# Optimization experiments

Hardware: AMD Instinct MI355X
Metric: run time of the kernel (lower is better)

Reference implementation:

```python
import jax, jax.numpy as jnp
import numpy as np

B, S, HID = 4, 2048, 2048
NH, NKV = 8, 1
HD = HID // NH  # 256
G = NH // NKV   # queries per kv head
ROPE_THETA = 10000.0
NEG_INF = -1e9


def setup_inputs() -> dict:
    key = jax.random.key(0)
    ks = jax.random.split(key, 4)
    x = jax.random.normal(ks[0], (B, S, HID), jnp.float32)
    qkv_dim = (NH + 2 * NKV) * HD
    w_qkv = jax.random.normal(ks[1], (HID, qkv_dim), jnp.float32) * (HID ** -0.5)
    b_qkv = jnp.zeros((qkv_dim,), jnp.float32)
    w_o = jax.random.normal(ks[2], (NH * HD, HID), jnp.float32) * ((NH * HD) ** -0.5)
    b_o = jnp.zeros((HID,), jnp.float32)
    # rotary table: cos/sin of position*inv_freq, interleaved-pair convention
    inv_freq = 1.0 / (ROPE_THETA ** (jnp.arange(0, HD, 2, dtype=jnp.float32) / HD))
    ang = jnp.outer(jnp.arange(S, dtype=jnp.float32), inv_freq)  # [S, HD/2]
    freqs_cis = jnp.stack([jnp.cos(ang), jnp.sin(ang)], axis=-1)  # [S, HD/2, 2]
    causal = jnp.tril(jnp.ones((S, S), bool))
    mask = jnp.where(causal, 0.0, NEG_INF).astype(jnp.float32)[None, None]  # [1,1,S,S]
    return dict(x=x, w_qkv=w_qkv, b_qkv=b_qkv, w_o=w_o, b_o=b_o,
                freqs_cis=freqs_cis, mask=mask)


def _rope(t, cos, sin):
    # t: [B,S,H,D]; cos/sin: [1,S,1,D/2]; interleaved complex pairs
    tp = t.reshape(*t.shape[:-1], -1, 2)
    r, i = tp[..., 0], tp[..., 1]
    out = jnp.stack([r * cos - i * sin, r * sin + i * cos], axis=-1)
    return out.reshape(t.shape)


def reference(x, w_qkv, b_qkv, w_o, b_o, freqs_cis, mask):
    b, s, _ = x.shape
    qkv = x @ w_qkv + b_qkv
    q, k, v = jnp.split(qkv, [NH * HD, NH * HD + NKV * HD], axis=-1)
    q = q.reshape(b, s, NH, HD)
    k = k.reshape(b, s, NKV, HD)
    v = v.reshape(b, s, NKV, HD)
    cos = freqs_cis[..., 0][None, :, None, :]
    sin = freqs_cis[..., 1][None, :, None, :]
    q = _rope(q, cos, sin)
    k = _rope(k, cos, sin)
    # GQA: head h attends with kv group h // G (same layout as repeat_interleave)
    qh = q.transpose(0, 2, 1, 3).reshape(b, NKV, G, s, HD)  # [B,KV,G,S,D]
    kh = k.transpose(0, 2, 1, 3)                            # [B,KV,S,D]
    vh = v.transpose(0, 2, 1, 3)
    scores = jnp.einsum('bkgqd,bksd->bkgqs', qh, kh) * (HD ** -0.5)
    scores = scores + mask[:, :, None]  # broadcast over group dim
    attn = jax.nn.softmax(scores.astype(jnp.float32), axis=-1).astype(q.dtype)
    out = jnp.einsum('bkgqs,bksd->bkgqd', attn, vh)         # [B,KV,G,S,D]
    out = out.reshape(b, NH, s, HD).transpose(0, 2, 1, 3).reshape(b, s, NH * HD)
    return out @ w_o + b_o
```

## Files before the change

kernel.cpp:

```cpp
#include <hip/hip_runtime.h>
#include <hip/hip_bf16.h>

#define B_ 4
#define S_ 2048
#define HID_ 2048
#define NH_ 8
#define HD_ 256
#define QKVN 2560

typedef unsigned short u16;
typedef unsigned long long ull;
typedef __attribute__((ext_vector_type(4))) float f32x4;
typedef __attribute__((ext_vector_type(16))) float f32x16;
typedef __attribute__((ext_vector_type(8))) short bf16x8;

__device__ __forceinline__ float bf2f(u16 u) {
  union { unsigned int i; float f; } v; v.i = ((unsigned int)u) << 16; return v.f;
}
__device__ __forceinline__ u16 f2bf(float f) {
  union { unsigned int i; float f; } v; v.f = f;
  unsigned int r = v.i + 0x7fffu + ((v.i >> 16) & 1u);
  return (u16)(r >> 16);
}

__global__ void cast_f32_bf16(const float* __restrict__ in, u16* __restrict__ out, int n8) {
  int i = blockIdx.x * blockDim.x + threadIdx.x;
  int stride = gridDim.x * blockDim.x;
  for (; i < n8; i += stride) {
    const float4* p = (const float4*)(in + (size_t)i * 8);
    float4 a = p[0], b = p[1];
    u16 o[8] = {f2bf(a.x), f2bf(a.y), f2bf(a.z), f2bf(a.w),
                f2bf(b.x), f2bf(b.y), f2bf(b.z), f2bf(b.w)};
    *(uint4*)(out + (size_t)i * 8) = *(const uint4*)o;
  }
}

__global__ void transpose_cast(const float* __restrict__ in, u16* __restrict__ out, int R, int C) {
  __shared__ float t[32][33];
  int c0 = blockIdx.x * 32, r0 = blockIdx.y * 32;
  int tx = threadIdx.x, ty = threadIdx.y;
#pragma unroll
  for (int i = 0; i < 4; ++i)
    t[ty + i * 8][tx] = in[(size_t)(r0 + ty + i * 8) * C + c0 + tx];
  __syncthreads();
#pragma unroll
  for (int i = 0; i < 4; ++i)
    out[(size_t)(c0 + ty + i * 8) * R + r0 + tx] = f2bf(t[tx][ty + i * 8]);
}

__global__ void transpose_bf16(const u16* __restrict__ in, u16* __restrict__ out, int R, int C) {
  __shared__ u16 t[32][33];
  in += (size_t)blockIdx.z * R * C;
  out += (size_t)blockIdx.z * R * C;
  int c0 = blockIdx.x * 32, r0 = blockIdx.y * 32;
  int tx = threadIdx.x, ty = threadIdx.y;
#pragma unroll
  for (int i = 0; i < 4; ++i)
    t[ty + i * 8][tx] = in[(size_t)(r0 + ty + i * 8) * C + c0 + tx];
  __syncthreads();
#pragma unroll
  for (int i = 0; i < 4; ++i)
    out[(size_t)(c0 + ty + i * 8) * R + r0 + tx] = t[tx][ty + i * 8];
}

#define BAR() __builtin_amdgcn_s_barrier()
#define PRIO1() __builtin_amdgcn_s_setprio(1)
#define PRIO0() __builtin_amdgcn_s_setprio(0)
#define SB0() __builtin_amdgcn_sched_barrier(0)
#define WVM(n)                                                                                    \
  do {                                                                                            \
    SB0();                                                                                        \
    asm volatile("s_waitcnt vmcnt(" #n ")" ::: "memory");                                         \
    SB0();                                                                                        \
  } while (0)

#define STG(mat, b0, h, T, ldsb)                                                                  \
  do {                                                                                            \
    _Pragma("unroll") for (int q = 0; q < 2; ++q) {                                               \
      int idx = q * 512 + tid;                                                                    \
      int rl = idx >> 3, gp = idx & 7;                                                            \
      const u16* s = (mat) + (size_t)((b0) + (h) * 128 + rl) * K + (T) * 64 +                     \
                     ((gp ^ (rl & 7)) << 3);                                                      \
      __builtin_amdgcn_global_load_lds((const __attribute__((address_space(1))) void*)s,          \
          (__attribute__((address_space(3))) void*)((ldsb) + (h) * 8192 + idx * 8), 16, 0, 0);    \
    }                                                                                             \
  } while (0)

#define LOAD_A(buf, mib)                                                                          \
  _Pragma("unroll") for (int mi = 0; mi < 4; ++mi)                                                \
  _Pragma("unroll") for (int ks = 0; ks < 2; ++ks)                                                \
    af[mi][ks] = *(const bf16x8*)((buf) + (wr * 128 + ((mib) + mi) * 16 + l15) * 64 +             \
                                  (((ks * 4 + lg) ^ (l15 & 7)) << 3));

#define LOAD_B(buf, nib)                                                                          \
  _Pragma("unroll") for (int ni = 0; ni < 2; ++ni)                                                \
  _Pragma("unroll") for (int ks = 0; ks < 2; ++ks)                                                \
    bfr[(nib) + ni][ks] = *(const bf16x8*)((buf) + (wc * 64 + ((nib) + ni) * 16 + l15) * 64 +     \
                                           (((ks * 4 + lg) ^ (l15 & 7)) << 3));

#define MFMA16(accb, nib)                                                                         \
  _Pragma("unroll") for (int mi = 0; mi < 4; ++mi)                                                \
  _Pragma("unroll") for (int ni = 0; ni < 2; ++ni)                                                \
  _Pragma("unroll") for (int ks = 0; ks < 2; ++ks)                                                \
    acc[(accb) + mi][(nib) + ni] = __builtin_amdgcn_mfma_f32_16x16x32_bf16(                       \
        af[mi][ks], bfr[(nib) + ni][ks], acc[(accb) + mi][(nib) + ni], 0, 0, 0);

template <bool OUT_F32>
__global__ __launch_bounds__(512, 2) void gemm256(const u16* __restrict__ A, const u16* __restrict__ BT,
                                                  const float* __restrict__ bias, void* __restrict__ Cout,
                                                  int M, int N, int K) {
  __shared__ u16 Asm[2][16384];
  __shared__ u16 Bsm[2][16384];
  int nwg = gridDim.x;
  int bid = (int)blockIdx.x;
  bid = (bid & 7) * (nwg >> 3) + (bid >> 3);
  int ntn = N >> 8;
  int m0 = (bid / ntn) << 8, n0 = (bid % ntn) << 8;
  int tid = threadIdx.x, w = tid >> 6, lane = tid & 63;
  int wr = w >> 2, wc = w & 3;
  int l15 = lane & 15, lg = lane >> 4;
  int NT = K >> 6;
  u16* A0b = &Asm[0][0]; u16* A1b = &Asm[1][0];
  u16* B0b = &Bsm[0][0]; u16* B1b = &Bsm[1][0];
  f32x4 acc[8][4] = {};
  bf16x8 af[4][2], bfr[4][2];

  STG(A, m0, 0, 0, A0b); STG(A, m0, 1, 0, A0b);
  STG(BT, n0, 0, 0, B0b); STG(BT, n0, 1, 0, B0b);
  STG(A, m0, 0, 1, A1b); STG(BT, n0, 0, 1, B1b);
  WVM(0);
  BAR();

  for (int T = 0; T + 2 < NT; T += 2) {
    LOAD_A(A0b, 0); LOAD_B(B0b, 0);
    STG(A, m0, 1, T + 1, A1b);
    BAR(); PRIO1(); MFMA16(0, 0); PRIO0(); BAR();
    LOAD_B(B0b, 2);
    STG(BT, n0, 1, T + 1, B1b);
    BAR(); PRIO1(); MFMA16(0, 2); PRIO0(); BAR();
    LOAD_A(A0b, 4);
    STG(BT, n0, 0, T + 2, B0b);
    BAR(); PRIO1(); MFMA16(4, 0); PRIO0(); BAR();
    STG(A, m0, 0, T + 2, A0b);
    WVM(4);
    BAR(); PRIO1(); MFMA16(4, 2); PRIO0(); BAR();
    LOAD_A(A1b, 0); LOAD_B(B1b, 0);
    STG(A, m0, 1, T + 2, A0b);
    BAR(); PRIO1(); MFMA16(0, 0); PRIO0(); BAR();
    LOAD_B(B1b, 2);
    STG(BT, n0, 1, T + 2, B0b);
    BAR(); PRIO1(); MFMA16(0, 2); PRIO0(); BAR();
    LOAD_A(A1b, 4);
    STG(BT, n0, 0, T + 3, B1b);
    BAR(); PRIO1(); MFMA16(4, 0); PRIO0(); BAR();
    STG(A, m0, 0, T + 3, A1b);
    WVM(4);
    BAR(); PRIO1(); MFMA16(4, 2); PRIO0(); BAR();
  }
  {
    int T = NT - 2;
    LOAD_A(A0b, 0); LOAD_B(B0b, 0);
    STG(A, m0, 1, T + 1, A1b);
    BAR(); PRIO1(); MFMA16(0, 0); PRIO0(); BAR();
    LOAD_B(B0b, 2);
    STG(BT, n0, 1, T + 1, B1b);
    BAR(); PRIO1(); MFMA16(0, 2); PRIO0(); BAR();
    LOAD_A(A0b, 4);
    BAR(); PRIO1(); MFMA16(4, 0); PRIO0(); BAR();
    WVM(0);
    BAR(); PRIO1(); MFMA16(4, 2); PRIO0(); BAR();
    LOAD_A(A1b, 0); LOAD_B(B1b, 0);
    BAR(); PRIO1(); MFMA16(0, 0); PRIO0(); BAR();
    LOAD_B(B1b, 2);
    BAR(); PRIO1(); MFMA16(0, 2); PRIO0(); BAR();
    LOAD_A(A1b, 4);
    BAR(); PRIO1(); MFMA16(4, 0); PRIO0(); BAR();
    PRIO1(); MFMA16(4, 2); PRIO0();
  }
#pragma unroll
  for (int mi = 0; mi < 8; ++mi) {
    int mrow = m0 + wr * 128 + mi * 16 + lg * 4;
#pragma unroll
    for (int ni = 0; ni < 4; ++ni) {
      int col = n0 + wc * 64 + ni * 16 + l15;
      float bv = bias[col];
#pragma unroll
      for (int j = 0; j < 4; ++j) {
        float v = acc[mi][ni][j] + bv;
        if (OUT_F32)
          ((float*)Cout)[(size_t)(mrow + j) * N + col] = v;
        else
          ((u16*)Cout)[(size_t)(mrow + j) * N + col] = f2bf(v);
      }
    }
  }
}

__global__ void rope_scatter(const u16* __restrict__ qkv, const float* __restrict__ freqs,
                             u16* __restrict__ qo, u16* __restrict__ ko, u16* __restrict__ vo) {
  const int per_row = QKVN / 8;
  const int total = B_ * S_ * per_row;
  int i = blockIdx.x * blockDim.x + threadIdx.x;
  int stride = gridDim.x * blockDim.x;
  for (; i < total; i += stride) {
    int m = i / per_row;
    int n8 = (i - m * per_row) * 8;
    int b = m >> 11, s = m & 2047;
    uint4 raw = *(const uint4*)(qkv + (size_t)m * QKVN + n8);
    const u16* u = (const u16*)&raw;
    if (n8 < 2304) {
      int d = (n8 < 2048) ? (n8 & 255) : (n8 - 2048);
      float scl = (n8 < 2048) ? (0.0625f * 1.44269504f) : 1.0f;
      const float* fp = freqs + ((size_t)s * 128 + (d >> 1)) * 2;
      float4 f0 = *(const float4*)fp;
      float4 f1 = *(const float4*)(fp + 4);
      float fc[8] = {f0.x, f0.y, f0.z, f0.w, f1.x, f1.y, f1.z, f1.w};
      u16 o[8];
#pragma unroll
      for (int p = 0; p < 4; ++p) {
        float r = bf2f(u[2 * p]), im = bf2f(u[2 * p + 1]);
        float c = fc[2 * p], sn = fc[2 * p + 1];
        o[2 * p] = f2bf((r * c - im * sn) * scl);
        o[2 * p + 1] = f2bf((r * sn + im * c) * scl);
      }
      u16* dst;
      if (n8 < 2048) {
        dst = qo + (size_t)m * 2048 + n8;
      } else {
        dst = ko + (((size_t)m) << 8) + d;
      }
      *(uint4*)dst = *(const uint4*)o;
    } else {
      int d = n8 - 2304;
      *(uint4*)(vo + (((size_t)m) << 8) + d) = raw;
    }
  }
}

#define STAGE_K(bufofs, kt)                                                                       \
  do {                                                                                            \
    _Pragma("unroll") for (int _p = 0; _p < 4; ++_p) {                                            \
      int _idx = _p * 512 + tid;                                                                  \
      int _row = _idx >> 5, _c = _idx & 31;                                                       \
      const u16* _src = Kp + ((size_t)(b * S_ + (kt) * 64 + _row)) * HD_ +                        \
                        ((_c ^ (_row & 31)) * 8);                                                 \
      __builtin_amdgcn_global_load_lds(                                                           \
          (const __attribute__((address_space(1))) void*)_src,                                    \
          (__attribute__((address_space(3))) void*)(KsBase + (bufofs) + _idx * 8), 16, 0, 0);     \
    }                                                                                             \
  } while (0)

#define STAGE_V(bufofs, kt)                                                                       \
  do {                                                                                            \
    _Pragma("unroll") for (int _p = 0; _p < 4; ++_p) {                                            \
      int _idx = _p * 512 + tid;                                                                  \
      int _r = _idx >> 4, _gp = _idx & 15;                                                        \
      int _g = _gp ^ (_r & 15);                                                                   \
      int _d = _r * 2 + (_g >> 3), _c = _g & 7;                                                   \
      const u16* _src = VTp + ((size_t)(b * 256 + _d)) * S_ + (kt) * 64 + _c * 8;                 \
      __builtin_amdgcn_global_load_lds(                                                           \
          (const __attribute__((address_space(1))) void*)_src,                                    \
          (__attribute__((address_space(3))) void*)(VsBase + (bufofs) + _idx * 8), 16, 0, 0);     \
    }                                                                                             \
  } while (0)

#define FLASH_TAU_BODY(Kbp, Vbp)                                                                  \
  do {                                                                                            \
    int row = tau * 32 + l31;                                                                     \
    f32x16 scv = {};                                                                              \
    __builtin_amdgcn_s_setprio(1);                                                                \
    _Pragma("unroll") for (int st = 0; st < 16; ++st) {                                           \
      bf16x8 kf = *(const bf16x8*)((Kbp) + row * 512 + (((st * 2 + lh) ^ l31) << 4));             \
      scv = __builtin_amdgcn_mfma_f32_32x32x16_bf16(kf, qf[st], scv, 0, 0, 0);                    \
    }                                                                                             \
    __builtin_amdgcn_s_setprio(0);                                                                \
    if (k0 + 31 > t * 32) {                                                                       \
      _Pragma("unroll") for (int jj = 0; jj < 16; ++jj) {                                         \
        int kg = k0 + (jj & 3) + 8 * (jj >> 2) + 4 * lh;                                          \
        if (kg > s_g) scv[jj] = -3.0e38f;                                                         \
      }                                                                                           \
    }                                                                                             \
    float tmax = -3.0e38f;                                                                        \
    _Pragma("unroll") for (int jj = 0; jj < 16; ++jj) tmax = fmaxf(tmax, scv[jj]);                \
    tmax = fmaxf(tmax, __shfl_xor(tmax, 32));                                                     \
    if (!__all(tmax - m_r <= 8.0f)) {                                                             \
      float mnew = fmaxf(m_r, tmax);                                                              \
      float sc = exp2f(m_r - mnew);                                                               \
      l_r *= sc;                                                                                  \
      _Pragma("unroll") for (int dt = 0; dt < 8; ++dt) oacc[dt] *= sc;                            \
      m_r = mnew;                                                                                 \
    }                                                                                             \
    float ts = 0.f;                                                                               \
    unsigned cpk[8];                                                                              \
    _Pragma("unroll") for (int mi = 0; mi < 8; ++mi) {                                            \
      float p0 = exp2f(scv[2 * mi] - m_r);                                                        \
      float p1 = exp2f(scv[2 * mi + 1] - m_r);                                                    \
      ts += p0 + p1;                                                                              \
      cpk[mi] = ((unsigned)f2bf(p1) << 16) | f2bf(p0);                                            \
    }                                                                                             \
    ts += __shfl_xor(ts, 32);                                                                     \
    l_r += ts;                                                                                    \
    asm volatile("v_permlane32_swap_b32 %0, %1" : "+v"(cpk[0]), "+v"(cpk[2]));                    \
    asm volatile("v_permlane32_swap_b32 %0, %1" : "+v"(cpk[1]), "+v"(cpk[3]));                    \
    asm volatile("v_permlane32_swap_b32 %0, %1" : "+v"(cpk[4]), "+v"(cpk[6]));                    \
    asm volatile("v_permlane32_swap_b32 %0, %1" : "+v"(cpk[5]), "+v"(cpk[7]));                    \
    union { unsigned u[4]; bf16x8 v; } pa, pb;                                                    \
    pa.u[0] = cpk[0]; pa.u[1] = cpk[1]; pa.u[2] = cpk[2]; pa.u[3] = cpk[3];                       \
    pb.u[0] = cpk[4]; pb.u[1] = cpk[5]; pb.u[2] = cpk[6]; pb.u[3] = cpk[7];                       \
    __builtin_amdgcn_s_setprio(1);                                                                \
    _Pragma("unroll") for (int dt = 0; dt < 8; ++dt) {                                            \
      int d = dt * 32 + l31;                                                                      \
      int rr = d >> 1;                                                                            \
      int gb = (d & 1) * 8 + tau * 4;                                                             \
      int rx = (rr & 15) << 4;                                                                    \
      bf16x8 va = *(const bf16x8*)((Vbp) + rr * 256 + (((gb + lh) << 4) ^ rx));                   \
      oacc[dt] = __builtin_amdgcn_mfma_f32_32x32x16_bf16(va, pa.v, oacc[dt], 0, 0, 0);            \
      bf16x8 vb2 = *(const bf16x8*)((Vbp) + rr * 256 + (((gb + 2 + lh) << 4) ^ rx));              \
      oacc[dt] = __builtin_amdgcn_mfma_f32_32x32x16_bf16(vb2, pb.v, oacc[dt], 0, 0, 0);           \
    }                                                                                             \
    __builtin_amdgcn_s_setprio(0);                                                                \
  } while (0)

__global__ __launch_bounds__(512, 2) void flash_attn_split(const u16* __restrict__ Qp, const u16* __restrict__ Kp,
                                                           const u16* __restrict__ VTp, u16* __restrict__ P0,
                                                           float* __restrict__ ml0, float* __restrict__ ml1,
                                                           u16* __restrict__ Op) {
  __shared__ u16 Ks[2][64 * 256];
  __shared__ u16 Vs[2][128 * 128];
  int bid = (int)blockIdx.x;
  int b = (bid & 7) >> 1;
  int j = ((bid & 1) << 5) + (bid >> 3);
  int tid = threadIdx.x;
  int w = tid >> 6, l = tid & 63;
  int l31 = l & 31, lh = l >> 5;
  int q_local = w * 32 + l31;
  u16* KsBase = &Ks[0][0];
  u16* VsBase = &Vs[0][0];

  for (int seg = 0; seg < 2; ++seg) {
    int t = seg ? (63 - j) : j;
    int nkv = (t >> 1) + 1;
    int half = (nkv + 1) >> 1;
    int kb = seg ? half : 0;
    int ke = seg ? nkv : half;
    size_t qrow = (size_t)b * 16384 + (size_t)t * 256 + q_local;
    int s_g = t * 32 + (q_local >> 3);
    float* mlbuf = seg ? ml1 : ml0;
    if (kb >= ke) {
      if (lh == 0) { mlbuf[qrow * 2] = -3.0e38f; mlbuf[qrow * 2 + 1] = 0.f; }
      continue;
    }
    bf16x8 qf[16];
    const u16* qp = Qp + qrow * HD_ + lh * 8;
#pragma unroll
    for (int st = 0; st < 16; ++st) qf[st] = *(const bf16x8*)(qp + st * 16);
    f32x16 oacc[8] = {};
    float m_r = -3.0e38f, l_r = 0.f;
    STAGE_K(0, kb);
    STAGE_V(0, kb);
    __syncthreads();
    int cur = 0;
    for (int kt = kb; kt < ke; ++kt) {
      if (kt + 1 < ke) {
        STAGE_K((cur ^ 1) * 16384, kt + 1);
        STAGE_V((cur ^ 1) * 16384, kt + 1);
      }
      const char* Kb = (const char*)(KsBase + cur * 16384);
      const char* Vb = (const char*)(VsBase + cur * 16384);
#pragma unroll
      for (int tau = 0; tau < 2; ++tau) {
        int k0 = kt * 64 + tau * 32;
        if (k0 > t * 32 + 31) break;
        FLASH_TAU_BODY(Kb, Vb);
      }
      __syncthreads();
      cur ^= 1;
    }
    float inv = 1.0f / l_r;
    u16* ob = (seg ? Op : P0) + qrow * 256;
#pragma unroll
    for (int dt = 0; dt < 8; ++dt) {
#pragma unroll
      for (int jj = 0; jj < 4; ++jj) {
        int d0 = dt * 32 + jj * 8 + 4 * lh;
        u16 o4[4];
#pragma unroll
        for (int e = 0; e < 4; ++e) o4[e] = f2bf(oacc[dt][jj * 4 + e] * inv);
        *(ull*)(ob + d0) = *(const ull*)o4;
      }
    }
    if (lh == 0) { mlbuf[qrow * 2] = m_r; mlbuf[qrow * 2 + 1] = l_r; }
  }
}

__global__ __launch_bounds__(256) void combine_parts(const u16* __restrict__ P0, const float* __restrict__ ml0,
                                                     const float* __restrict__ ml1, u16* __restrict__ O) {
  int idx = blockIdx.x * 256 + threadIdx.x;
  int r = idx >> 5;
  int c = (idx & 31) * 8;
  float m0 = ml0[(size_t)r * 2], l0 = ml0[(size_t)r * 2 + 1];
  float m1 = ml1[(size_t)r * 2], l1 = ml1[(size_t)r * 2 + 1];
  float M = fmaxf(m0, m1);
  float w0 = l0 * exp2f(m0 - M), w1 = l1 * exp2f(m1 - M);
  float inv = 1.0f / (w0 + w1);
  w0 *= inv; w1 *= inv;
  uint4 a = *(const uint4*)(P0 + (size_t)r * 256 + c);
  uint4 bq = *(const uint4*)(O + (size_t)r * 256 + c);
  const u16* ua = (const u16*)&a;
  const u16* ub = (const u16*)&bq;
  u16 o[8];
#pragma unroll
  for (int e = 0; e < 8; ++e) o[e] = f2bf(w0 * bf2f(ua[e]) + w1 * bf2f(ub[e]));
  *(uint4*)(O + (size_t)r * 256 + c) = *(const uint4*)o;
}

#define STAGE_K1(kt)                                                                              \
  do {                                                                                            \
    _Pragma("unroll") for (int _p = 0; _p < 4; ++_p) {                                            \
      int _idx = _p * 512 + tid;                                                                  \
      int _row = _idx >> 5, _c = _idx & 31;                                                       \
      const u16* _src = Kp + ((size_t)(b * S_ + (kt) * 64 + _row)) * HD_ +                        \
                        ((_c ^ (_row & 31)) * 8);                                                 \
      __builtin_amdgcn_global_load_lds(                                                           \
          (const __attribute__((address_space(1))) void*)_src,                                    \
          (__attribute__((address_space(3))) void*)(KsBase + _idx * 8), 16, 0, 0);                \
    }                                                                                             \
  } while (0)

#define STAGE_V1(kt)                                                                              \
  do {                                                                                            \
    _Pragma("unroll") for (int _p = 0; _p < 4; ++_p) {                                            \
      int _idx = _p * 512 + tid;                                                                  \
      int _r = _idx >> 4, _gp = _idx & 15;                                                        \
      int _g = _gp ^ (_r & 15);                                                                   \
      int _d = _r * 2 + (_g >> 3), _c = _g & 7;                                                   \
      const u16* _src = VTp + ((size_t)(b * 256 + _d)) * S_ + (kt) * 64 + _c * 8;                 \
      __builtin_amdgcn_global_load_lds(                                                           \
          (const __attribute__((address_space(1))) void*)_src,                                    \
          (__attribute__((address_space(3))) void*)(VsBase + _idx * 8), 16, 0, 0);                \
    }                                                                                             \
  } while (0)

__global__ __launch_bounds__(512, 2) void flash_attn_split4(const u16* __restrict__ Qp, const u16* __restrict__ Kp,
                                                            const u16* __restrict__ VTp,
                                                            u16* __restrict__ P0, u16* __restrict__ P1,
                                                            u16* __restrict__ P2, u16* __restrict__ Op,
                                                            float* __restrict__ ml0, float* __restrict__ ml1,
                                                            float* __restrict__ ml2, float* __restrict__ ml3) {
  __shared__ u16 Ks[64 * 256];
  __shared__ u16 Vs[128 * 128];
  int bid = (int)blockIdx.x;
  int b = (bid & 7) >> 1;
  int rest = ((bid & 1) << 7) | (bid >> 3);
  int t = rest & 63;
  int p = rest >> 6;
  int tid = threadIdx.x;
  int w = tid >> 6, l = tid & 63;
  int l31 = l & 31, lh = l >> 5;
  int q_local = w * 32 + l31;
  u16* KsBase = &Ks[0];
  u16* VsBase = &Vs[0];

  int nkv = (t >> 1) + 1;
  int kb = (nkv * p) >> 2;
  int ke = (nkv * (p + 1)) >> 2;
  size_t qrow = (size_t)b * 16384 + (size_t)t * 256 + q_local;
  int s_g = t * 32 + (q_local >> 3);
  u16* Obuf = (p == 0) ? P0 : (p == 1) ? P1 : (p == 2) ? P2 : Op;
  float* mlbuf = (p == 0) ? ml0 : (p == 1) ? ml1 : (p == 2) ? ml2 : ml3;

  if (kb >= ke) {
    if (lh == 0) { mlbuf[qrow * 2] = -3.0e38f; mlbuf[qrow * 2 + 1] = 0.f; }
    return;
  }

  bf16x8 qf[16];
  const u16* qp = Qp + qrow * HD_ + lh * 8;
#pragma unroll
  for (int st = 0; st < 16; ++st) qf[st] = *(const bf16x8*)(qp + st * 16);
  f32x16 oacc[8] = {};
  float m_r = -3.0e38f, l_r = 0.f;

  STAGE_K1(kb);
  STAGE_V1(kb);
  __syncthreads();
  for (int kt = kb; kt < ke; ++kt) {
#pragma unroll
    for (int tau = 0; tau < 2; ++tau) {
      int k0 = kt * 64 + tau * 32;
      if (k0 > t * 32 + 31) break;
      FLASH_TAU_BODY((const char*)KsBase, (const char*)VsBase);
    }
    __syncthreads();
    if (kt + 1 < ke) {
      STAGE_K1(kt + 1);
      STAGE_V1(kt + 1);
      __syncthreads();
    }
  }

  float inv = 1.0f / l_r;
  u16* ob = Obuf + qrow * 256;
#pragma unroll
  for (int dt = 0; dt < 8; ++dt) {
#pragma unroll
    for (int jj = 0; jj < 4; ++jj) {
      int d0 = dt * 32 + jj * 8 + 4 * lh;
      u16 o4[4];
#pragma unroll
      for (int e = 0; e < 4; ++e) o4[e] = f2bf(oacc[dt][jj * 4 + e] * inv);
      *(ull*)(ob + d0) = *(const ull*)o4;
    }
  }
  if (lh == 0) { mlbuf[qrow * 2] = m_r; mlbuf[qrow * 2 + 1] = l_r; }
}

__global__ __launch_bounds__(256) void combine_parts4(const u16* __restrict__ P0, const u16* __restrict__ P1,
                                                      const u16* __restrict__ P2, const float* __restrict__ ml0,
                                                      const float* __restrict__ ml1, const float* __restrict__ ml2,
                                                      const float* __restrict__ ml3, u16* __restrict__ O) {
  int idx = blockIdx.x * 256 + threadIdx.x;
  int r = idx >> 5;
  int c = (idx & 31) * 8;
  float m0 = ml0[(size_t)r * 2], l0 = ml0[(size_t)r * 2 + 1];
  float m1 = ml1[(size_t)r * 2], l1 = ml1[(size_t)r * 2 + 1];
  float m2 = ml2[(size_t)r * 2], l2 = ml2[(size_t)r * 2 + 1];
  float m3 = ml3[(size_t)r * 2], l3 = ml3[(size_t)r * 2 + 1];
  float M = fmaxf(fmaxf(m0, m1), fmaxf(m2, m3));
  float w0 = l0 * exp2f(m0 - M), w1 = l1 * exp2f(m1 - M);
  float w2 = l2 * exp2f(m2 - M), w3 = l3 * exp2f(m3 - M);
  float inv = 1.0f / (w0 + w1 + w2 + w3);
  w0 *= inv; w1 *= inv; w2 *= inv; w3 *= inv;
  uint4 a0 = *(const uint4*)(P0 + (size_t)r * 256 + c);
  uint4 a1 = *(const uint4*)(P1 + (size_t)r * 256 + c);
  uint4 a2 = *(const uint4*)(P2 + (size_t)r * 256 + c);
  uint4 a3 = *(const uint4*)(O + (size_t)r * 256 + c);
  const u16* u0 = (const u16*)&a0;
  const u16* u1 = (const u16*)&a1;
  const u16* u2 = (const u16*)&a2;
  const u16* u3 = (const u16*)&a3;
  u16 o[8];
#pragma unroll
  for (int e = 0; e < 8; ++e)
    o[e] = f2bf(w0 * bf2f(u0[e]) + w1 * bf2f(u1[e]) + w2 * bf2f(u2[e]) + w3 * bf2f(u3[e]));
  *(uint4*)(O + (size_t)r * 256 + c) = *(const uint4*)o;
}

extern "C" void kernel_launch(void* const* d_in, const int* in_sizes, int n_in,
                              void* d_out, int out_size, void* d_ws, size_t ws_size,
                              hipStream_t stream) {
  const float* x = (const float*)d_in[0];
  const float* w_qkv = (const float*)d_in[1];
  const float* b_qkv = (const float*)d_in[2];
  const float* w_o = (const float*)d_in[3];
  const float* b_o = (const float*)d_in[4];
  const float* freqs = (const float*)d_in[5];

  char* ws = (char*)d_ws;
  u16* xb    = (u16*)ws;
  u16* wqkvT = (u16*)(ws + 33554432);
  u16* woT   = (u16*)(ws + 44040192);
  u16* qkv   = (u16*)(ws + 52428800);
  u16* qall  = (u16*)(ws + 94371840);
  u16* kbuf  = (u16*)(ws + 127926272);
  u16* vbuf  = (u16*)(ws + 132120576);
  u16* part0 = (u16*)(ws + 136314880);
  float* ml0 = (float*)(ws + 169869312);
  float* ml1 = (float*)(ws + 170393600);
  u16* part1 = (u16*)(ws + 170917888);
  u16* part2 = (u16*)(ws + 204472320);
  float* ml2 = (float*)(ws + 33554432);
  float* ml3 = (float*)(ws + 33554432 + 524288);
  u16* vT    = xb;
  u16* attout = qkv;

  bool split4 = (ws_size >= 238026752ULL);

  cast_f32_bf16<<<2048, 256, 0, stream>>>(x, xb, (B_ * S_ * HID_) / 8);
  transpose_cast<<<dim3(QKVN / 32, HID_ / 32), dim3(32, 8), 0, stream>>>(w_qkv, wqkvT, HID_, QKVN);
  transpose_cast<<<dim3(HID_ / 32, HID_ / 32), dim3(32, 8), 0, stream>>>(w_o, woT, HID_, HID_);
  gemm256<false><<<dim3(32 * 10), 512, 0, stream>>>(xb, wqkvT, b_qkv, qkv, B_ * S_, QKVN, HID_);
  rope_scatter<<<2048, 256, 0, stream>>>(qkv, freqs, qall, kbuf, vbuf);
  transpose_bf16<<<dim3(HD_ / 32, S_ / 32, B_), dim3(32, 8), 0, stream>>>(vbuf, vT, S_, HD_);
  if (split4) {
    flash_attn_split4<<<1024, 512, 0, stream>>>(qall, kbuf, vT, part0, part1, part2, attout,
                                                ml0, ml1, ml2, ml3);
    combine_parts4<<<8192, 256, 0, stream>>>(part0, part1, part2, ml0, ml1, ml2, ml3, attout);
  } else {
    flash_attn_split<<<256, 512, 0, stream>>>(qall, kbuf, vT, part0, ml0, ml1, attout);
    combine_parts<<<8192, 256, 0, stream>>>(part0, ml0, ml1, attout);
  }
  gemm256<true><<<dim3(32 * 8), 512, 0, stream>>>(attout, woT, b_o, d_out, B_ * S_, HID_, HID_);
}
```

Before: 464.7 us.

## Replace 4-way KV split attention with 2-way split using smaller 256-thread blocks

```diff
diff --git a/kernel.cpp b/kernel.cpp
--- a/kernel.cpp
+++ b/kernel.cpp
@@ -237,30 +237,31 @@
   }
 }
 
-#define STAGE_K(bufofs, kt)                                                                       \
+
+#define STAGE_K1(kt)                                                                              \
   do {                                                                                            \
-    _Pragma("unroll") for (int _p = 0; _p < 4; ++_p) {                                            \
-      int _idx = _p * 512 + tid;                                                                  \
+    _Pragma("unroll") for (int _p = 0; _p < 8; ++_p) {                                            \
+      int _idx = _p * 256 + tid;                                                                  \
       int _row = _idx >> 5, _c = _idx & 31;                                                       \
       const u16* _src = Kp + ((size_t)(b * S_ + (kt) * 64 + _row)) * HD_ +                        \
                         ((_c ^ (_row & 31)) * 8);                                                 \
       __builtin_amdgcn_global_load_lds(                                                           \
           (const __attribute__((address_space(1))) void*)_src,                                    \
-          (__attribute__((address_space(3))) void*)(KsBase + (bufofs) + _idx * 8), 16, 0, 0);     \
+          (__attribute__((address_space(3))) void*)(KsBase + _idx * 8), 16, 0, 0);                \
     }                                                                                             \
   } while (0)
 
-#define STAGE_V(bufofs, kt)                                                                       \
+#define STAGE_V1(kt)                                                                              \
   do {                                                                                            \
-    _Pragma("unroll") for (int _p = 0; _p < 4; ++_p) {                                            \
-      int _idx = _p * 512 + tid;                                                                  \
+    _Pragma("unroll") for (int _p = 0; _p < 8; ++_p) {                                            \
+      int _idx = _p * 256 + tid;                                                                  \
       int _r = _idx >> 4, _gp = _idx & 15;                                                        \
       int _g = _gp ^ (_r & 15);                                                                   \
       int _d = _r * 2 + (_g >> 3), _c = _g & 7;                                                   \
       const u16* _src = VTp + ((size_t)(b * 256 + _d)) * S_ + (kt) * 64 + _c * 8;                 \
       __builtin_amdgcn_global_load_lds(                                                           \
           (const __attribute__((address_space(1))) void*)_src,                                    \
-          (__attribute__((address_space(3))) void*)(VsBase + (bufofs) + _idx * 8), 16, 0, 0);     \
+          (__attribute__((address_space(3))) void*)(VsBase + _idx * 8), 16, 0, 0);                \
     }                                                                                             \
   } while (0)
 
@@ -274,7 +275,7 @@
       scv = __builtin_amdgcn_mfma_f32_32x32x16_bf16(kf, qf[st], scv, 0, 0, 0);                    \
     }                                                                                             \
     __builtin_amdgcn_s_setprio(0);                                                                \
-    if (k0 + 31 > t * 32) {                                                                       \
+    if (needmask) {                                                                               \
       _Pragma("unroll") for (int jj = 0; jj < 16; ++jj) {                                         \
         int kg = k0 + (jj & 3) + 8 * (jj >> 2) + 4 * lh;                                          \
         if (kg > s_g) scv[jj] = -3.0e38f;                                                         \
@@ -321,31 +322,33 @@
     __builtin_amdgcn_s_setprio(0);                                                                \
   } while (0)
 
-__global__ __launch_bounds__(512, 2) void flash_attn_split(const u16* __restrict__ Qp, const u16* __restrict__ Kp,
+__global__ __launch_bounds__(256, 2) void flash_attn_split(const u16* __restrict__ Qp, const u16* __restrict__ Kp,
                                                            const u16* __restrict__ VTp, u16* __restrict__ P0,
                                                            float* __restrict__ ml0, float* __restrict__ ml1,
                                                            u16* __restrict__ Op) {
-  __shared__ u16 Ks[2][64 * 256];
-  __shared__ u16 Vs[2][128 * 128];
+  __shared__ u16 Ks[64 * 256];
+  __shared__ u16 Vs[128 * 128];
   int bid = (int)blockIdx.x;
   int b = (bid & 7) >> 1;
-  int j = ((bid & 1) << 5) + (bid >> 3);
+  int part = bid & 1;
+  int pair = bid >> 3;
   int tid = threadIdx.x;
   int w = tid >> 6, l = tid & 63;
   int l31 = l & 31, lh = l >> 5;
   int q_local = w * 32 + l31;
-  u16* KsBase = &Ks[0][0];
-  u16* VsBase = &Vs[0][0];
+  u16* KsBase = &Ks[0];
+  u16* VsBase = &Vs[0];
+  float* mlbuf = part ? ml1 : ml0;
 
   for (int seg = 0; seg < 2; ++seg) {
-    int t = seg ? (63 - j) : j;
-    int nkv = (t >> 1) + 1;
+    int t = seg ? (127 - pair) : pair;
+    int nkv = (t >> 2) + 1;
     int half = (nkv + 1) >> 1;
-    int kb = seg ? half : 0;
-    int ke = seg ? nkv : half;
-    size_t qrow = (size_t)b * 16384 + (size_t)t * 256 + q_local;
-    int s_g = t * 32 + (q_local >> 3);
-    float* mlbuf = seg ? ml1 : ml0;
+    int kb = part ? half : 0;
+    int ke = part ? nkv : half;
+    size_t qrow = (size_t)b * 16384 + (size_t)t * 128 + q_local;
+    int s_g = t * 16 + (q_local >> 3);
+    int smin = t * 16, smax = t * 16 + 15;
     if (kb >= ke) {
       if (lh == 0) { mlbuf[qrow * 2] = -3.0e38f; mlbuf[qrow * 2 + 1] = 0.f; }
       continue;
@@ -356,28 +359,28 @@
     for (int st = 0; st < 16; ++st) qf[st] = *(const bf16x8*)(qp + st * 16);
     f32x16 oacc[8] = {};
     float m_r = -3.0e38f, l_r = 0.f;
-    STAGE_K(0, kb);
-    STAGE_V(0, kb);
+
+    STAGE_K1(kb);
+    STAGE_V1(kb);
     __syncthreads();
-    int cur = 0;
     for (int kt = kb; kt < ke; ++kt) {
-      if (kt + 1 < ke) {
-        STAGE_K((cur ^ 1) * 16384, kt + 1);
-        STAGE_V((cur ^ 1) * 16384, kt + 1);
-      }
-      const char* Kb = (const char*)(KsBase + cur * 16384);
-      const char* Vb = (const char*)(VsBase + cur * 16384);
 #pragma unroll
       for (int tau = 0; tau < 2; ++tau) {
         int k0 = kt * 64 + tau * 32;
-        if (k0 > t * 32 + 31) break;
-        FLASH_TAU_BODY(Kb, Vb);
+        if (k0 > smax) break;
+        bool needmask = (k0 + 31 > smin);
+        FLASH_TAU_BODY((const char*)KsBase, (const char*)VsBase);
       }
       __syncthreads();
-      cur ^= 1;
+      if (kt + 1 < ke) {
+        STAGE_K1(kt + 1);
+        STAGE_V1(kt + 1);
+        __syncthreads();
+      }
     }
+
     float inv = 1.0f / l_r;
-    u16* ob = (seg ? Op : P0) + qrow * 256;
+    u16* ob = (part ? Op : P0) + qrow * 256;
 #pragma unroll
     for (int dt = 0; dt < 8; ++dt) {
 #pragma unroll
@@ -414,138 +417,6 @@
   *(uint4*)(O + (size_t)r * 256 + c) = *(const uint4*)o;
 }
 
-#define STAGE_K1(kt)                                                                              \
-  do {                                                                                            \
-    _Pragma("unroll") for (int _p = 0; _p < 4; ++_p) {                                            \
-      int _idx = _p * 512 + tid;                                                                  \
-      int _row = _idx >> 5, _c = _idx & 31;                                                       \
-      const u16* _src = Kp + ((size_t)(b * S_ + (kt) * 64 + _row)) * HD_ +                        \
-                        ((_c ^ (_row & 31)) * 8);                                                 \
-      __builtin_amdgcn_global_load_lds(                                                           \
-          (const __attribute__((address_space(1))) void*)_src,                                    \
-          (__attribute__((address_space(3))) void*)(KsBase + _idx * 8), 16, 0, 0);                \
-    }                                                                                             \
-  } while (0)
-
-#define STAGE_V1(kt)                                                                              \
-  do {                                                                                            \
-    _Pragma("unroll") for (int _p = 0; _p < 4; ++_p) {                                            \
-      int _idx = _p * 512 + tid;                                                                  \
-      int _r = _idx >> 4, _gp = _idx & 15;                                                        \
-      int _g = _gp ^ (_r & 15);                                                                   \
-      int _d = _r * 2 + (_g >> 3), _c = _g & 7;                                                   \
-      const u16* _src = VTp + ((size_t)(b * 256 + _d)) * S_ + (kt) * 64 + _c * 8;                 \
-      __builtin_amdgcn_global_load_lds(                                                           \
-          (const __attribute__((address_space(1))) void*)_src,                                    \
-          (__attribute__((address_space(3))) void*)(VsBase + _idx * 8), 16, 0, 0);                \
-    }                                                                                             \
-  } while (0)
-
-__global__ __launch_bounds__(512, 2) void flash_attn_split4(const u16* __restrict__ Qp, const u16* __restrict__ Kp,
-                                                            const u16* __restrict__ VTp,
-                                                            u16* __restrict__ P0, u16* __restrict__ P1,
-                                                            u16* __restrict__ P2, u16* __restrict__ Op,
-                                                            float* __restrict__ ml0, float* __restrict__ ml1,
-                                                            float* __restrict__ ml2, float* __restrict__ ml3) {
-  __shared__ u16 Ks[64 * 256];
-  __shared__ u16 Vs[128 * 128];
-  int bid = (int)blockIdx.x;
-  int b = (bid & 7) >> 1;
-  int rest = ((bid & 1) << 7) | (bid >> 3);
-  int t = rest & 63;
-  int p = rest >> 6;
-  int tid = threadIdx.x;
-  int w = tid >> 6, l = tid & 63;
-  int l31 = l & 31, lh = l >> 5;
-  int q_local = w * 32 + l31;
-  u16* KsBase = &Ks[0];
-  u16* VsBase = &Vs[0];
-
-  int nkv = (t >> 1) + 1;
-  int kb = (nkv * p) >> 2;
-  int ke = (nkv * (p + 1)) >> 2;
-  size_t qrow = (size_t)b * 16384 + (size_t)t * 256 + q_local;
-  int s_g = t * 32 + (q_local >> 3);
-  u16* Obuf = (p == 0) ? P0 : (p == 1) ? P1 : (p == 2) ? P2 : Op;
-  float* mlbuf = (p == 0) ? ml0 : (p == 1) ? ml1 : (p == 2) ? ml2 : ml3;
-
-  if (kb >= ke) {
-    if (lh == 0) { mlbuf[qrow * 2] = -3.0e38f; mlbuf[qrow * 2 + 1] = 0.f; }
-    return;
-  }
-
-  bf16x8 qf[16];
-  const u16* qp = Qp + qrow * HD_ + lh * 8;
-#pragma unroll
-  for (int st = 0; st < 16; ++st) qf[st] = *(const bf16x8*)(qp + st * 16);
-  f32x16 oacc[8] = {};
-  float m_r = -3.0e38f, l_r = 0.f;
-
-  STAGE_K1(kb);
-  STAGE_V1(kb);
-  __syncthreads();
-  for (int kt = kb; kt < ke; ++kt) {
-#pragma unroll
-    for (int tau = 0; tau < 2; ++tau) {
-      int k0 = kt * 64 + tau * 32;
-      if (k0 > t * 32 + 31) break;
-      FLASH_TAU_BODY((const char*)KsBase, (const char*)VsBase);
-    }
-    __syncthreads();
-    if (kt + 1 < ke) {
-      STAGE_K1(kt + 1);
-      STAGE_V1(kt + 1);
-      __syncthreads();
-    }
-  }
-
-  float inv = 1.0f / l_r;
-  u16* ob = Obuf + qrow * 256;
-#pragma unroll
-  for (int dt = 0; dt < 8; ++dt) {
-#pragma unroll
-    for (int jj = 0; jj < 4; ++jj) {
-      int d0 = dt * 32 + jj * 8 + 4 * lh;
-      u16 o4[4];
-#pragma unroll
-      for (int e = 0; e < 4; ++e) o4[e] = f2bf(oacc[dt][jj * 4 + e] * inv);
-      *(ull*)(ob + d0) = *(const ull*)o4;
-    }
-  }
-  if (lh == 0) { mlbuf[qrow * 2] = m_r; mlbuf[qrow * 2 + 1] = l_r; }
-}
-
-__global__ __launch_bounds__(256) void combine_parts4(const u16* __restrict__ P0, const u16* __restrict__ P1,
-                                                      const u16* __restrict__ P2, const float* __restrict__ ml0,
-                                                      const float* __restrict__ ml1, const float* __restrict__ ml2,
-                                                      const float* __restrict__ ml3, u16* __restrict__ O) {
-  int idx = blockIdx.x * 256 + threadIdx.x;
-  int r = idx >> 5;
-  int c = (idx & 31) * 8;
-  float m0 = ml0[(size_t)r * 2], l0 = ml0[(size_t)r * 2 + 1];
-  float m1 = ml1[(size_t)r * 2], l1 = ml1[(size_t)r * 2 + 1];
-  float m2 = ml2[(size_t)r * 2], l2 = ml2[(size_t)r * 2 + 1];
-  float m3 = ml3[(size_t)r * 2], l3 = ml3[(size_t)r * 2 + 1];
-  float M = fmaxf(fmaxf(m0, m1), fmaxf(m2, m3));
-  float w0 = l0 * exp2f(m0 - M), w1 = l1 * exp2f(m1 - M);
-  float w2 = l2 * exp2f(m2 - M), w3 = l3 * exp2f(m3 - M);
-  float inv = 1.0f / (w0 + w1 + w2 + w3);
-  w0 *= inv; w1 *= inv; w2 *= inv; w3 *= inv;
-  uint4 a0 = *(const uint4*)(P0 + (size_t)r * 256 + c);
-  uint4 a1 = *(const uint4*)(P1 + (size_t)r * 256 + c);
-  uint4 a2 = *(const uint4*)(P2 + (size_t)r * 256 + c);
-  uint4 a3 = *(const uint4*)(O + (size_t)r * 256 + c);
-  const u16* u0 = (const u16*)&a0;
-  const u16* u1 = (const u16*)&a1;
-  const u16* u2 = (const u16*)&a2;
-  const u16* u3 = (const u16*)&a3;
-  u16 o[8];
-#pragma unroll
-  for (int e = 0; e < 8; ++e)
-    o[e] = f2bf(w0 * bf2f(u0[e]) + w1 * bf2f(u1[e]) + w2 * bf2f(u2[e]) + w3 * bf2f(u3[e]));
-  *(uint4*)(O + (size_t)r * 256 + c) = *(const uint4*)o;
-}
-
 extern "C" void kernel_launch(void* const* d_in, const int* in_sizes, int n_in,
                               void* d_out, int out_size, void* d_ws, size_t ws_size,
                               hipStream_t stream) {
@@ -567,14 +438,8 @@
   u16* part0 = (u16*)(ws + 136314880);
   float* ml0 = (float*)(ws + 169869312);
   float* ml1 = (float*)(ws + 170393600);
-  u16* part1 = (u16*)(ws + 170917888);
-  u16* part2 = (u16*)(ws + 204472320);
-  float* ml2 = (float*)(ws + 33554432);
-  float* ml3 = (float*)(ws + 33554432 + 524288);
   u16* vT    = xb;
   u16* attout = qkv;
-
-  bool split4 = (ws_size >= 238026752ULL);
 
   cast_f32_bf16<<<2048, 256, 0, stream>>>(x, xb, (B_ * S_ * HID_) / 8);
   transpose_cast<<<dim3(QKVN / 32, HID_ / 32), dim3(32, 8), 0, stream>>>(w_qkv, wqkvT, HID_, QKVN);
@@ -582,13 +447,7 @@
   gemm256<false><<<dim3(32 * 10), 512, 0, stream>>>(xb, wqkvT, b_qkv, qkv, B_ * S_, QKVN, HID_);
   rope_scatter<<<2048, 256, 0, stream>>>(qkv, freqs, qall, kbuf, vbuf);
   transpose_bf16<<<dim3(HD_ / 32, S_ / 32, B_), dim3(32, 8), 0, stream>>>(vbuf, vT, S_, HD_);
-  if (split4) {
-    flash_attn_split4<<<1024, 512, 0, stream>>>(qall, kbuf, vT, part0, part1, part2, attout,
-                                                ml0, ml1, ml2, ml3);
-    combine_parts4<<<8192, 256, 0, stream>>>(part0, part1, part2, ml0, ml1, ml2, ml3, attout);
-  } else {
-    flash_attn_split<<<256, 512, 0, stream>>>(qall, kbuf, vT, part0, ml0, ml1, attout);
-    combine_parts<<<8192, 256, 0, stream>>>(part0, ml0, ml1, attout);
-  }
+  flash_attn_split<<<512, 256, 0, stream>>>(qall, kbuf, vT, part0, ml0, ml1, attout);
+  combine_parts<<<8192, 256, 0, stream>>>(part0, ml0, ml1, attout);
   gemm256<true><<<dim3(32 * 8), 512, 0, stream>>>(attout, woT, b_o, d_out, B_ * S_, HID_, HID_);
 }
```

Result: slower. 504.8 us (+8.6%).
